# Kernel tuning notes

Hardware: AMD Instinct MI355X
Metric: run time of the kernel (lower is better)

## Reference

```python
import jax, jax.numpy as jnp
import numpy as np

B, SQ, SK, H, A = 4, 512, 512, 256, 128

def setup_inputs() -> dict:
    key = jax.random.key(0)
    ks = jax.random.split(key, 8)
    s = 1.0 / np.sqrt(H)
    sa = 1.0 / np.sqrt(A)
    return {
        "Q": jax.random.normal(ks[0], (B, SQ, H), dtype=jnp.float32),
        "K": jax.random.normal(ks[1], (B, SK, H), dtype=jnp.float32),
        "V": jax.random.normal(ks[2], (B, SK, H), dtype=jnp.float32),
        "W_q": jax.random.uniform(ks[3], (H, A), jnp.float32, -s, s),
        "W_k": jax.random.uniform(ks[4], (H, A), jnp.float32, -s, s),
        "v": jax.random.uniform(ks[5], (A,), jnp.float32, -sa, sa),
        "W_o": jax.random.uniform(ks[6], (H, H), jnp.float32, -s, s),
        "b_o": jax.random.uniform(ks[7], (H,), jnp.float32, -s, s),
    }

def reference(Q, K, V, W_q, W_k, v, W_o, b_o):
    # Q: (B, Sq, H), K/V: (B, Sk, H)
    Qt = Q @ W_q                      # (B, Sq, A)
    Kt = K @ W_k                      # (B, Sk, A)
    additive = jnp.tanh(Qt[:, :, None, :] + Kt[:, None, :, :])  # (B, Sq, Sk, A)
    scores = jnp.einsum('bqka,a->bqk', additive, v)             # (B, Sq, Sk)
    weights = jax.nn.softmax(scores, axis=-1)                   # (B, Sq, Sk)
    out = jnp.einsum('bqk,bkh->bqh', weights, V)                 # (B, Sq, H)
    out = out @ W_o + b_o
    return (out, weights)
```

## Files before the change

kernel.cpp:

```cpp
#include <hip/hip_runtime.h>
#include <math.h>

#define BB 4
#define SQL 512
#define SKL 512
#define HH 256
#define AA 128

#define PRESCALE 2.8853900817779268f
#define LOG2E    1.4426950408889634f

__device__ inline void fma4(float4& a, float s, const float4& b) {
    a.x = fmaf(s, b.x, a.x); a.y = fmaf(s, b.y, a.y);
    a.z = fmaf(s, b.z, a.z); a.w = fmaf(s, b.w, a.w);
}

template <int CTRL>
__device__ __forceinline__ float dpp_add(float x) {
    int m = __builtin_amdgcn_update_dpp(__float_as_int(x), __float_as_int(x),
                                        CTRL, 0xF, 0xF, false);
    return x + __int_as_float(m);
}
__device__ __forceinline__ float red16(float x) {
    x = dpp_add<0xB1>(x);
    x = dpp_add<0x4E>(x);
    x = dpp_add<0x141>(x);
    x = dpp_add<0x140>(x);
    return x;
}

__global__ __launch_bounds__(256) void prep_kernel(
    const float* __restrict__ Q, const float* __restrict__ K,
    const float* __restrict__ V,
    const float* __restrict__ Wq, const float* __restrict__ Wk,
    const float* __restrict__ Wo,
    float* __restrict__ Qt, float* __restrict__ Kt, float* __restrict__ VW)
{
    __shared__ float rows[16 * HH];
    __shared__ float wl[64 * 128];
    int tid = threadIdx.x;
    int bid = blockIdx.x;

    const float* X; const float* W; float* Y;
    int ldW, ldY, col0, r0; float scale;
    if (bid < 128)      { X=Q; W=Wq; Y=Qt; ldW=AA; ldY=AA; col0=0; r0=bid*16;       scale=PRESCALE; }
    else if (bid < 256) { X=K; W=Wk; Y=Kt; ldW=AA; ldY=AA; col0=0; r0=(bid-128)*16; scale=PRESCALE; }
    else { int b2=bid-256; X=V; W=Wo; Y=VW; ldW=HH; ldY=HH; col0=(b2&1)*128; r0=(b2>>1)*16; scale=1.0f; }

    {
        const float4* Xv = (const float4*)(X + (size_t)r0 * HH);
        float4* rv = (float4*)rows;
        rv[tid]       = Xv[tid];
        rv[tid + 256] = Xv[tid + 256];
        rv[tid + 512] = Xv[tid + 512];
        rv[tid + 768] = Xv[tid + 768];
    }

    int r  = tid >> 5;
    int c4 = tid & 31;
    float4 accA = {0.f,0.f,0.f,0.f}, accB = {0.f,0.f,0.f,0.f};

    for (int ch = 0; ch < 4; ++ch) {
        __syncthreads();
        {
            const float* Wbase = W + (size_t)(ch * 64) * ldW + col0;
            float4* wv = (float4*)wl;
            #pragma unroll
            for (int it = 0; it < 8; ++it) {
                int l = tid + it * 256;
                wv[l] = *(const float4*)(Wbase + (size_t)(l >> 5) * ldW + ((l & 31) << 2));
            }
        }
        __syncthreads();
        const float* rrowA = rows + r * HH + ch * 64;
        const float* rrowB = rows + (r + 8) * HH + ch * 64;
        #pragma unroll 4
        for (int h4 = 0; h4 < 16; ++h4) {
            float4 ra = *(const float4*)(rrowA + h4 * 4);
            float4 rb = *(const float4*)(rrowB + h4 * 4);
            const float* wbase = wl + (h4 * 4) * 128 + (c4 << 2);
            float4 w0 = *(const float4*)(wbase);
            float4 w1 = *(const float4*)(wbase + 128);
            float4 w2 = *(const float4*)(wbase + 256);
            float4 w3 = *(const float4*)(wbase + 384);
            fma4(accA, ra.x, w0); fma4(accA, ra.y, w1);
            fma4(accA, ra.z, w2); fma4(accA, ra.w, w3);
            fma4(accB, rb.x, w0); fma4(accB, rb.y, w1);
            fma4(accB, rb.z, w2); fma4(accB, rb.w, w3);
        }
    }
    accA.x *= scale; accA.y *= scale; accA.z *= scale; accA.w *= scale;
    accB.x *= scale; accB.y *= scale; accB.z *= scale; accB.w *= scale;
    *(float4*)(Y + (size_t)(r0 + r)     * ldY + col0 + (c4 << 2)) = accA;
    *(float4*)(Y + (size_t)(r0 + r + 8) * ldY + col0 + (c4 << 2)) = accB;
}

#define FORQ(OP) OP(0) OP(1) OP(2) OP(3) OP(4) OP(5) OP(6) OP(7)

__global__ __launch_bounds__(512)
__attribute__((amdgpu_waves_per_eu(2, 2)))
void score_kernel(
    const float* __restrict__ Qt, const float* __restrict__ Kt,
    const float* __restrict__ v,  const float* __restrict__ VW,
    const float* __restrict__ bo,
    float* __restrict__ weights,  float* __restrict__ out)
{
    __shared__ float score[8][SKL];
    __shared__ float pout[8][4][HH];

    int tid = threadIdx.x;
    int b  = blockIdx.x >> 6;
    int q0 = (blockIdx.x & 63) << 3;
    int ag = tid & 15;
    int kl = tid >> 4;

    float4 v2a, v2b;
    {
        const float4* vp = (const float4*)(v + ag * 8);
        v2a = vp[0]; v2b = vp[1];
        v2a.x *= 2.f; v2a.y *= 2.f; v2a.z *= 2.f; v2a.w *= 2.f;
        v2b.x *= 2.f; v2b.y *= 2.f; v2b.z *= 2.f; v2b.w *= 2.f;
    }

#define DECL_EQ(Qi) float4 EqA##Qi, EqB##Qi;
    FORQ(DECL_EQ)
#define LOAD_EQ(Qi) { \
        const float4* qp = (const float4*)(Qt + (size_t)(b * SQL + q0 + Qi) * AA + ag * 8); \
        float4 t0 = qp[0], t1 = qp[1]; \
        (EqA##Qi).x = __builtin_amdgcn_exp2f(t0.x); (EqA##Qi).y = __builtin_amdgcn_exp2f(t0.y); \
        (EqA##Qi).z = __builtin_amdgcn_exp2f(t0.z); (EqA##Qi).w = __builtin_amdgcn_exp2f(t0.w); \
        (EqB##Qi).x = __builtin_amdgcn_exp2f(t1.x); (EqB##Qi).y = __builtin_amdgcn_exp2f(t1.y); \
        (EqB##Qi).z = __builtin_amdgcn_exp2f(t1.z); (EqB##Qi).w = __builtin_amdgcn_exp2f(t1.w); }
    FORQ(LOAD_EQ)

    float S_all;
    {
        float ls = (v2a.x + v2a.y) + (v2a.z + v2a.w)
                 + (v2b.x + v2b.y) + (v2b.z + v2b.w);
        S_all = 0.5f * red16(ls);
    }

    const float4* ktp = (const float4*)(Kt + (size_t)b * SKL * AA);

    {
        float4 ka = ktp[(size_t)kl * (AA / 4) + ag * 2];
        float4 kb = ktp[(size_t)kl * (AA / 4) + ag * 2 + 1];
        #pragma unroll 1
        for (int c = 0; c < 16; ++c) {
            float4 na, nb;
            if (c < 15) {
                int kn = (c + 1) * 32 + kl;
                na = ktp[(size_t)kn * (AA / 4) + ag * 2];
                nb = ktp[(size_t)kn * (AA / 4) + ag * 2 + 1];
            }
#define DECL_P(Qi) float p##Qi = 0.f;
            FORQ(DECL_P)
#define STEP(KE, VE, HB, COMP) { \
            float Ek = __builtin_amdgcn_exp2f(KE); \
            p0 = fmaf(VE, __builtin_amdgcn_rcpf(fmaf(Ek, (Eq##HB##0).COMP, 1.0f)), p0); \
            p1 = fmaf(VE, __builtin_amdgcn_rcpf(fmaf(Ek, (Eq##HB##1).COMP, 1.0f)), p1); \
            p2 = fmaf(VE, __builtin_amdgcn_rcpf(fmaf(Ek, (Eq##HB##2).COMP, 1.0f)), p2); \
            p3 = fmaf(VE, __builtin_amdgcn_rcpf(fmaf(Ek, (Eq##HB##3).COMP, 1.0f)), p3); \
            p4 = fmaf(VE, __builtin_amdgcn_rcpf(fmaf(Ek, (Eq##HB##4).COMP, 1.0f)), p4); \
            p5 = fmaf(VE, __builtin_amdgcn_rcpf(fmaf(Ek, (Eq##HB##5).COMP, 1.0f)), p5); \
            p6 = fmaf(VE, __builtin_amdgcn_rcpf(fmaf(Ek, (Eq##HB##6).COMP, 1.0f)), p6); \
            p7 = fmaf(VE, __builtin_amdgcn_rcpf(fmaf(Ek, (Eq##HB##7).COMP, 1.0f)), p7); }
            STEP(ka.x, v2a.x, A, x) STEP(ka.y, v2a.y, A, y)
            STEP(ka.z, v2a.z, A, z) STEP(ka.w, v2a.w, A, w)
            STEP(kb.x, v2b.x, B, x) STEP(kb.y, v2b.y, B, y)
            STEP(kb.z, v2b.z, B, z) STEP(kb.w, v2b.w, B, w)
#define RED_P(Qi) p##Qi = red16(p##Qi);
            FORQ(RED_P)
            if (ag == 0) {
                int k = c * 32 + kl;
#define STORE_P(Qi) score[Qi][k] = (S_all - p##Qi) * LOG2E;
                FORQ(STORE_P)
            }
            ka = na; kb = nb;
        }
    }
    __syncthreads();

    int wave = tid >> 6, lane = tid & 63;
    {
        int qi = wave;
        float ssum = 0.f;
        #pragma unroll
        for (int it = 0; it < 2; ++it) {
            int k0 = it * 256 + (lane << 2);
            float4 sv = *(float4*)&score[qi][k0];
            sv.x = __builtin_amdgcn_exp2f(sv.x);
            sv.y = __builtin_amdgcn_exp2f(sv.y);
            sv.z = __builtin_amdgcn_exp2f(sv.z);
            sv.w = __builtin_amdgcn_exp2f(sv.w);
            *(float4*)&score[qi][k0] = sv;
            ssum += (sv.x + sv.y) + (sv.z + sv.w);
        }
        #pragma unroll
        for (int off = 32; off; off >>= 1) ssum += __shfl_xor(ssum, off);
        float rinv = 1.0f / ssum;
        size_t rowoff = (size_t)(b * SQL + q0 + qi) * SKL;
        #pragma unroll
        for (int it = 0; it < 2; ++it) {
            int k0 = it * 256 + (lane << 2);
            float4 sv = *(float4*)&score[qi][k0];
            sv.x *= rinv; sv.y *= rinv; sv.z *= rinv; sv.w *= rinv;
            *(float4*)&score[qi][k0] = sv;
            *(float4*)(weights + rowoff + k0) = sv;
        }
    }
    __syncthreads();

#define DECL_ACC(Qi) float4 acc##Qi = {0.f, 0.f, 0.f, 0.f};
    FORQ(DECL_ACC)
    {
        const float4* VWb = (const float4*)(VW + (size_t)b * SKL * HH);
        int kbase = wave * 64;
        #pragma unroll 2
        for (int k4 = 0; k4 < 16; ++k4) {
            int kk = kbase + k4 * 4;
#define DECL_W(Qi) float4 w##Qi = *(const float4*)&score[Qi][kk];
            FORQ(DECL_W)
            float4 vw;
            vw = VWb[(size_t)(kk + 0) * (HH / 4) + lane];
#define FMA_X(Qi) fma4(acc##Qi, (w##Qi).x, vw);
            FORQ(FMA_X)
            vw = VWb[(size_t)(kk + 1) * (HH / 4) + lane];
#define FMA_Y(Qi) fma4(acc##Qi, (w##Qi).y, vw);
            FORQ(FMA_Y)
            vw = VWb[(size_t)(kk + 2) * (HH / 4) + lane];
#define FMA_Z(Qi) fma4(acc##Qi, (w##Qi).z, vw);
            FORQ(FMA_Z)
            vw = VWb[(size_t)(kk + 3) * (HH / 4) + lane];
#define FMA_W(Qi) fma4(acc##Qi, (w##Qi).w, vw);
            FORQ(FMA_W)
        }
    }

    int h  = tid & 255;
    int qh = tid >> 8;
    float bias = bo[h];

    *(float4*)&pout[wave][0][lane << 2] = acc0;
    *(float4*)&pout[wave][1][lane << 2] = acc1;
    *(float4*)&pout[wave][2][lane << 2] = acc2;
    *(float4*)&pout[wave][3][lane << 2] = acc3;
    __syncthreads();
    #pragma unroll
    for (int qq = 0; qq < 2; ++qq) {
        int qi = qh * 2 + qq;
        float s = bias;
        #pragma unroll
        for (int w2 = 0; w2 < 8; ++w2) s += pout[w2][qi][h];
        out[(size_t)(b * SQL + q0 + qi) * HH + h] = s;
    }
    __syncthreads();

    *(float4*)&pout[wave][0][lane << 2] = acc4;
    *(float4*)&pout[wave][1][lane << 2] = acc5;
    *(float4*)&pout[wave][2][lane << 2] = acc6;
    *(float4*)&pout[wave][3][lane << 2] = acc7;
    __syncthreads();
    #pragma unroll
    for (int qq = 0; qq < 2; ++qq) {
        int qi = qh * 2 + qq;
        float s = bias;
        #pragma unroll
        for (int w2 = 0; w2 < 8; ++w2) s += pout[w2][qi][h];
        out[(size_t)(b * SQL + q0 + 4 + qi) * HH + h] = s;
    }
}

extern "C" void kernel_launch(void* const* d_in, const int* in_sizes, int n_in,
                              void* d_out, int out_size, void* d_ws, size_t ws_size,
                              hipStream_t stream)
{
    const float* Q  = (const float*)d_in[0];
    const float* K  = (const float*)d_in[1];
    const float* V  = (const float*)d_in[2];
    const float* Wq = (const float*)d_in[3];
    const float* Wk = (const float*)d_in[4];
    const float* v  = (const float*)d_in[5];
    const float* Wo = (const float*)d_in[6];
    const float* bo = (const float*)d_in[7];

    float* out     = (float*)d_out;
    float* weights = out + (size_t)BB * SQL * HH;

    float* Qt = (float*)d_ws;
    float* Kt = Qt + (size_t)BB * SQL * AA;
    float* VW = Kt + (size_t)BB * SKL * AA;

    prep_kernel <<<512, 256, 0, stream>>>(Q, K, V, Wq, Wk, Wo, Qt, Kt, VW);
    score_kernel<<<256, 512, 0, stream>>>(Qt, Kt, v, VW, bo, weights, out);
}
```

Baseline: 118.0 us.

## Batch reciprocals across query rows and precompute exp2 in projection GEMM

Applies exp2 to the projected Q and K values once, in the projection GEMM epilogue, instead of recomputing exp2 of each K element inside the score loop. It also replaces eight separate reciprocals per step with two, using a product tree where each row's reciprocal is recovered from shared products by multiplication. This trades transcendental-unit pressure for extra multiplies and more live registers. Multiplying four denominators together also risks overflow or precision loss when the exponentials are large.

```diff
diff --git a/kernel.cpp b/kernel.cpp
--- a/kernel.cpp
+++ b/kernel.cpp
@@ -91,6 +91,12 @@
     }
     accA.x *= scale; accA.y *= scale; accA.z *= scale; accA.w *= scale;
     accB.x *= scale; accB.y *= scale; accB.z *= scale; accB.w *= scale;
+    if (bid < 256) {
+        accA.x = __builtin_amdgcn_exp2f(accA.x); accA.y = __builtin_amdgcn_exp2f(accA.y);
+        accA.z = __builtin_amdgcn_exp2f(accA.z); accA.w = __builtin_amdgcn_exp2f(accA.w);
+        accB.x = __builtin_amdgcn_exp2f(accB.x); accB.y = __builtin_amdgcn_exp2f(accB.y);
+        accB.z = __builtin_amdgcn_exp2f(accB.z); accB.w = __builtin_amdgcn_exp2f(accB.w);
+    }
     *(float4*)(Y + (size_t)(r0 + r)     * ldY + col0 + (c4 << 2)) = accA;
     *(float4*)(Y + (size_t)(r0 + r + 8) * ldY + col0 + (c4 << 2)) = accB;
 }
@@ -126,11 +132,7 @@
     FORQ(DECL_EQ)
 #define LOAD_EQ(Qi) { \
         const float4* qp = (const float4*)(Qt + (size_t)(b * SQL + q0 + Qi) * AA + ag * 8); \
-        float4 t0 = qp[0], t1 = qp[1]; \
-        (EqA##Qi).x = __builtin_amdgcn_exp2f(t0.x); (EqA##Qi).y = __builtin_amdgcn_exp2f(t0.y); \
-        (EqA##Qi).z = __builtin_amdgcn_exp2f(t0.z); (EqA##Qi).w = __builtin_amdgcn_exp2f(t0.w); \
-        (EqB##Qi).x = __builtin_amdgcn_exp2f(t1.x); (EqB##Qi).y = __builtin_amdgcn_exp2f(t1.y); \
-        (EqB##Qi).z = __builtin_amdgcn_exp2f(t1.z); (EqB##Qi).w = __builtin_amdgcn_exp2f(t1.w); }
+        (EqA##Qi) = qp[0]; (EqB##Qi) = qp[1]; }
     FORQ(LOAD_EQ)
 
     float S_all;
@@ -155,20 +157,34 @@
             }
 #define DECL_P(Qi) float p##Qi = 0.f;
             FORQ(DECL_P)
-#define STEP(KE, VE, HB, COMP) { \
-            float Ek = __builtin_amdgcn_exp2f(KE); \
-            p0 = fmaf(VE, __builtin_amdgcn_rcpf(fmaf(Ek, (Eq##HB##0).COMP, 1.0f)), p0); \
-            p1 = fmaf(VE, __builtin_amdgcn_rcpf(fmaf(Ek, (Eq##HB##1).COMP, 1.0f)), p1); \
-            p2 = fmaf(VE, __builtin_amdgcn_rcpf(fmaf(Ek, (Eq##HB##2).COMP, 1.0f)), p2); \
-            p3 = fmaf(VE, __builtin_amdgcn_rcpf(fmaf(Ek, (Eq##HB##3).COMP, 1.0f)), p3); \
-            p4 = fmaf(VE, __builtin_amdgcn_rcpf(fmaf(Ek, (Eq##HB##4).COMP, 1.0f)), p4); \
-            p5 = fmaf(VE, __builtin_amdgcn_rcpf(fmaf(Ek, (Eq##HB##5).COMP, 1.0f)), p5); \
-            p6 = fmaf(VE, __builtin_amdgcn_rcpf(fmaf(Ek, (Eq##HB##6).COMP, 1.0f)), p6); \
-            p7 = fmaf(VE, __builtin_amdgcn_rcpf(fmaf(Ek, (Eq##HB##7).COMP, 1.0f)), p7); }
-            STEP(ka.x, v2a.x, A, x) STEP(ka.y, v2a.y, A, y)
-            STEP(ka.z, v2a.z, A, z) STEP(ka.w, v2a.w, A, w)
-            STEP(kb.x, v2b.x, B, x) STEP(kb.y, v2b.y, B, y)
-            STEP(kb.z, v2b.z, B, z) STEP(kb.w, v2b.w, B, w)
+#define STEPC(KE, VE, HB, COMP) { \
+            float Ek = KE; \
+            float d0 = fmaf(Ek, (Eq##HB##0).COMP, 1.0f); \
+            float d1 = fmaf(Ek, (Eq##HB##1).COMP, 1.0f); \
+            float d2 = fmaf(Ek, (Eq##HB##2).COMP, 1.0f); \
+            float d3 = fmaf(Ek, (Eq##HB##3).COMP, 1.0f); \
+            float d4 = fmaf(Ek, (Eq##HB##4).COMP, 1.0f); \
+            float d5 = fmaf(Ek, (Eq##HB##5).COMP, 1.0f); \
+            float d6 = fmaf(Ek, (Eq##HB##6).COMP, 1.0f); \
+            float d7 = fmaf(Ek, (Eq##HB##7).COMP, 1.0f); \
+            float m01 = d0 * d1, m23 = d2 * d3; \
+            float m45 = d4 * d5, m67 = d6 * d7; \
+            float t03 = __builtin_amdgcn_rcpf(m01 * m23); \
+            float t47 = __builtin_amdgcn_rcpf(m45 * m67); \
+            float rm01 = t03 * m23, rm23 = t03 * m01; \
+            float rm45 = t47 * m67, rm67 = t47 * m45; \
+            p0 = fmaf(VE, rm01 * d1, p0); \
+            p1 = fmaf(VE, rm01 * d0, p1); \
+            p2 = fmaf(VE, rm23 * d3, p2); \
+            p3 = fmaf(VE, rm23 * d2, p3); \
+            p4 = fmaf(VE, rm45 * d5, p4); \
+            p5 = fmaf(VE, rm45 * d4, p5); \
+            p6 = fmaf(VE, rm67 * d7, p6); \
+            p7 = fmaf(VE, rm67 * d6, p7); }
+            STEPC(ka.x, v2a.x, A, x) STEPC(ka.y, v2a.y, A, y)
+            STEPC(ka.z, v2a.z, A, z) STEPC(ka.w, v2a.w, A, w)
+            STEPC(kb.x, v2b.x, B, x) STEPC(kb.y, v2b.y, B, y)
+            STEPC(kb.z, v2b.z, B, z) STEPC(kb.w, v2b.w, B, w)
 #define RED_P(Qi) p##Qi = red16(p##Qi);
             FORQ(RED_P)
             if (ag == 0) {
```

Result: no change. 119.3 us (+1.1%).
